# Optimization experiments

Hardware: AMD Instinct MI355X
Metric: run time of the kernel (lower is better)

Reference implementation:

```python
import jax, jax.numpy as jnp
import numpy as np

C = 384; H = 32; W = 32; HEADS = 12; HD = C // HEADS; MLP = 1536
KOFF = 5; OFF_RANGE = 2.0


def layer_norm(x, g, b, eps=1e-5):
    mu = jnp.mean(x, axis=-1, keepdims=True)
    var = jnp.mean(jnp.square(x - mu), axis=-1, keepdims=True)
    return (x - mu) * jax.lax.rsqrt(var + eps) * g + b


def depthwise_conv(x, k):
    # x: (B,H,W,C), k: (kh,kw,1,C), SAME padding, groups=C
    return jax.lax.conv_general_dilated(
        x, k, window_strides=(1, 1), padding='SAME',
        dimension_numbers=('NHWC', 'HWIO', 'NHWC'), feature_group_count=C)


def grid_sample_bilinear(img, pos):
    # img: (B,H,W,C); pos: (B,H,W,2) normalized (y,x) in [-1,1], align_corners=True, border clamp
    B, Hh, Ww, Cc = img.shape
    py = (pos[..., 0] + 1.0) * 0.5 * (Hh - 1)
    px = (pos[..., 1] + 1.0) * 0.5 * (Ww - 1)
    y0 = jnp.floor(py); x0 = jnp.floor(px)
    wy = (py - y0)[..., None]; wx = (px - x0)[..., None]
    y0i = jnp.clip(y0.astype(jnp.int32), 0, Hh - 1)
    y1i = jnp.clip(y0i + 1, 0, Hh - 1)
    x0i = jnp.clip(x0.astype(jnp.int32), 0, Ww - 1)
    x1i = jnp.clip(x0i + 1, 0, Ww - 1)
    b = jnp.arange(B)[:, None, None]
    g = lambda yi, xi: img[b, yi, xi]
    return (g(y0i, x0i) * (1 - wy) * (1 - wx) + g(y0i, x1i) * (1 - wy) * wx
            + g(y1i, x0i) * wy * (1 - wx) + g(y1i, x1i) * wy * wx)


def setup_inputs() -> dict:
    key = jax.random.key(0)
    ks = jax.random.split(key, 16)
    n = jax.random.normal
    s = 0.02
    inp = {
        'x': n(ks[0], (16, H * W, C), jnp.float32),
        'ln1_g': jnp.ones((C,), jnp.float32), 'ln1_b': jnp.zeros((C,), jnp.float32),
        'Wq': n(ks[1], (C, C), jnp.float32) * s, 'bq': jnp.zeros((C,), jnp.float32),
        'off_k': n(ks[2], (KOFF, KOFF, 1, C), jnp.float32) * s,
        'off_kb': jnp.zeros((C,), jnp.float32),
        'offln_g': jnp.ones((C,), jnp.float32), 'offln_b': jnp.zeros((C,), jnp.float32),
        'Woff': n(ks[3], (2, C), jnp.float32) * s, 'boff': jnp.zeros((2,), jnp.float32),
        'Wk': n(ks[4], (C, C), jnp.float32) * s, 'bk': jnp.zeros((C,), jnp.float32),
        'Wv': n(ks[5], (C, C), jnp.float32) * s, 'bv': jnp.zeros((C,), jnp.float32),
        'Wo': n(ks[6], (C, C), jnp.float32) * s, 'bo': jnp.zeros((C,), jnp.float32),
        'ln2_g': jnp.ones((C,), jnp.float32), 'ln2_b': jnp.zeros((C,), jnp.float32),
        'W1': n(ks[7], (MLP, C), jnp.float32) * s, 'b1': jnp.zeros((MLP,), jnp.float32),
        'W2': n(ks[8], (C, MLP), jnp.float32) * s, 'b2': jnp.zeros((C,), jnp.float32),
    }
    return inp


def _block(x, ln1_g, ln1_b, Wq, bq, off_k, off_kb, offln_g, offln_b, Woff, boff,
           Wk, bk, Wv, bv, Wo, bo, ln2_g, ln2_b, W1, b1, W2, b2):
    B, N, _ = x.shape
    # --- deformable attention branch ---
    xn = layer_norm(x, ln1_g, ln1_b)
    xi = xn.reshape(B, H, W, C)
    q = xi @ Wq.T + bq                                  # (B,H,W,C)
    # offset network: depthwise conv -> LN -> GELU -> 1x1 conv to 2
    off = depthwise_conv(q, off_k) + off_kb
    off = jax.nn.gelu(layer_norm(off, offln_g, offln_b))
    off = off @ Woff.T + boff                           # (B,H,W,2)
    off_range = jnp.array([OFF_RANGE * 2.0 / H, OFF_RANGE * 2.0 / W], jnp.float32)
    off = jnp.tanh(off) * off_range                     # normalized coord units
    ry = (jnp.arange(H, dtype=jnp.float32) + 0.5) / H * 2.0 - 1.0
    rx = (jnp.arange(W, dtype=jnp.float32) + 0.5) / W * 2.0 - 1.0
    ref = jnp.stack(jnp.meshgrid(ry, rx, indexing='ij'), axis=-1)  # (H,W,2)
    pos = ref[None] + off                               # (B,H,W,2)
    xs = grid_sample_bilinear(xi, pos).reshape(B, N, C)  # sampled keys/values source
    k = xs @ Wk.T + bk
    v = xs @ Wv.T + bv
    qh = q.reshape(B, N, HEADS, HD).transpose(0, 2, 1, 3)
    kh = k.reshape(B, N, HEADS, HD).transpose(0, 2, 1, 3)
    vh = v.reshape(B, N, HEADS, HD).transpose(0, 2, 1, 3)
    attn = jax.nn.softmax(jnp.einsum('bhqd,bhkd->bhqk', qh, kh) * (HD ** -0.5), axis=-1)
    o = jnp.einsum('bhqk,bhkd->bhqd', attn, vh).transpose(0, 2, 1, 3).reshape(B, N, C)
    x = x + (o @ Wo.T + bo)
    # --- MLP branch ---
    y = layer_norm(x, ln2_g, ln2_b)
    y = jax.nn.gelu(y @ W1.T + b1) @ W2.T + b2
    return x + y


def reference(x, ln1_g, ln1_b, Wq, bq, off_k, off_kb, offln_g, offln_b, Woff, boff,
              Wk, bk, Wv, bv, Wo, bo, ln2_g, ln2_b, W1, b1, W2, b2):
    return _block(x, ln1_g, ln1_b, Wq, bq, off_k, off_kb, offln_g, offln_b, Woff, boff,
                  Wk, bk, Wv, bv, Wo, bo, ln2_g, ln2_b, W1, b1, W2, b2)
```

## Files before the change

### kernel.cpp

```cpp
#include <hip/hip_runtime.h>
#include <math.h>

#define DI __device__ __forceinline__

typedef __attribute__((ext_vector_type(8))) short bf16x8;
typedef __attribute__((ext_vector_type(4))) float f32x4;

static constexpr int CC = 384;
static constexpr float QSCALE = 0.17677669529663687f * 1.4426950408889634f;
static constexpr float INVQS  = 1.0f / QSCALE;

DI unsigned short f2bf(float f){
  unsigned u = __float_as_uint(f);
  u += 0x7FFFu + ((u >> 16) & 1u);
  return (unsigned short)(u >> 16);
}
DI float bf2f(unsigned short u){ return __uint_as_float((unsigned)u << 16); }
DI float lo16(unsigned u){ return __uint_as_float(u << 16); }
DI float hi16(unsigned u){ return __uint_as_float(u & 0xFFFF0000u); }
DI float fexp2(float x){ return __builtin_amdgcn_exp2f(x); }
DI float frcp(float x){ return __builtin_amdgcn_rcpf(x); }
DI float tanh_fast(float z){ return 1.f - 2.f*frcp(fexp2(2.8853900817779268f*z) + 1.f); }
DI float gelu_fast(float v){
  float u = v*v;
  float z = 0.7978845608028654f * fmaf(0.044715f*u, v, v);
  return v - v*frcp(fexp2(2.8853900817779268f*z) + 1.f);
}
DI f32x4 mfma16(bf16x8 a, bf16x8 b, f32x4 c){
  return __builtin_amdgcn_mfma_f32_16x16x32_bf16(a, b, c, 0, 0, 0);
}
DI void gload16(const unsigned short* g, unsigned short* l){
  __builtin_amdgcn_global_load_lds(
      (const __attribute__((address_space(1))) unsigned int*)(const void*)g,
      (__attribute__((address_space(3))) unsigned int*)(void*)l, 16, 0, 0);
}

__global__ __launch_bounds__(256) void k_cvt_all(
    const float* __restrict__ wq, const float* __restrict__ wk,
    const float* __restrict__ wv, const float* __restrict__ wo,
    const float* __restrict__ w1, const float* __restrict__ w2,
    const float* __restrict__ ofk,
    unsigned short* __restrict__ dst)
{
  int i4 = (blockIdx.x*256 + threadIdx.x)*4;
  if (i4 >= 1779072) return;
  const float* src; int off;
  if (i4 < 147456){ src = wq; off = i4; }
  else if (i4 < 294912){ src = wk; off = i4 - 147456; }
  else if (i4 < 442368){ src = wv; off = i4 - 294912; }
  else if (i4 < 589824){ src = wo; off = i4 - 442368; }
  else if (i4 < 1179648){ src = w1; off = i4 - 589824; }
  else if (i4 < 1769472){ src = w2; off = i4 - 1179648; }
  else { src = ofk; off = i4 - 1769472; }
  float4 v = *(const float4*)(src + off);
  uint2 o;
  o.x = ((unsigned)f2bf(v.y) << 16) | f2bf(v.x);
  o.y = ((unsigned)f2bf(v.w) << 16) | f2bf(v.z);
  *(uint2*)(dst + i4) = o;
}

template<int BIN>
__global__ __launch_bounds__(256) void k_ln(const float* __restrict__ xf,
    const unsigned short* __restrict__ xb,
    const float* __restrict__ g, const float* __restrict__ b,
    unsigned short* __restrict__ outb)
{
  int row = blockIdx.x*4 + (threadIdx.x >> 6);
  int l = threadIdx.x & 63;
  float v[6]; int ch[6];
  if constexpr (BIN){
    int cA = 4*l, cB = 256 + 2*l;
    ch[0]=cA; ch[1]=cA+1; ch[2]=cA+2; ch[3]=cA+3; ch[4]=cB; ch[5]=cB+1;
    const unsigned short* xp = xb + (size_t)row * CC;
    uint2 u2 = *(const uint2*)(xp + cA);
    unsigned u1 = *(const unsigned*)(xp + cB);
    v[0]=lo16(u2.x); v[1]=hi16(u2.x); v[2]=lo16(u2.y); v[3]=hi16(u2.y);
    v[4]=lo16(u1);   v[5]=hi16(u1);
  } else {
    const float* xp = xf + (size_t)row * CC;
#pragma unroll
    for (int p = 0; p < 6; p++){ ch[p] = l + 64*p; v[p] = xp[ch[p]]; }
  }
  float s = 0.f, s2 = 0.f;
#pragma unroll
  for (int p = 0; p < 6; p++){ s += v[p]; s2 += v[p]*v[p]; }
#pragma unroll
  for (int m = 32; m; m >>= 1){ s += __shfl_xor(s, m); s2 += __shfl_xor(s2, m); }
  float mu = s * (1.f/CC);
  float var = s2 * (1.f/CC) - mu*mu;
  float rs = rsqrtf(var + 1e-5f);
  float o[6];
#pragma unroll
  for (int p = 0; p < 6; p++) o[p] = (v[p] - mu) * rs * g[ch[p]] + b[ch[p]];
  unsigned short* op = outb + (size_t)row*CC;
  if constexpr (BIN){
    uint2 st;
    st.x = ((unsigned)f2bf(o[1]) << 16) | f2bf(o[0]);
    st.y = ((unsigned)f2bf(o[3]) << 16) | f2bf(o[2]);
    *(uint2*)(op + ch[0]) = st;
    *(unsigned*)(op + ch[4]) = ((unsigned)f2bf(o[5]) << 16) | f2bf(o[4]);
  } else {
#pragma unroll
    for (int p = 0; p < 6; p++) op[ch[p]] = f2bf(o[p]);
  }
}

template<int EPI>
__global__ __launch_bounds__(256) void k_gemm64(
    const unsigned short* __restrict__ A, const unsigned short* __restrict__ W,
    const float* __restrict__ bias, const float* __restrict__ bias2,
    const float* __restrict__ res, const unsigned short* __restrict__ resb,
    float* __restrict__ outf, unsigned short* __restrict__ outb,
    unsigned short* __restrict__ outb2, int ntn, int N, int K)
{
  __shared__ unsigned short As[2][2048];
  __shared__ unsigned short Bs[2][4096];
  int bid = blockIdx.x;
  int cpx = gridDim.x >> 3;
  int id = (bid & 7)*cpx + (bid >> 3);
  int bn = (id % ntn) * 128;
  int bm = (id / ntn) * 64;
  int t = threadIdx.x;
  int w = t >> 6, l = t & 63;
  int g = l >> 4, ln = l & 15;
  int wm = w >> 1, wn = w & 1;
  f32x4 acc[2][4];
#pragma unroll
  for (int i = 0; i < 2; i++)
#pragma unroll
    for (int j = 0; j < 4; j++) acc[i][j] = (f32x4){0.f,0.f,0.f,0.f};
  int srow = t >> 2, slot = t & 3;
  int srowB = srow + 64;
  int cb0 = (slot ^ (srow  & 3) ^ ((srow  >> 2) & 3)) * 8;
  int cb1 = (slot ^ (srowB & 3) ^ ((srowB >> 2) & 3)) * 8;
  const unsigned short* Ap  = A + (size_t)(bm + srow)*K + cb0;
  const unsigned short* Wp0 = W + (size_t)(bn + srow)*K + cb0;
  const unsigned short* Wp1 = W + (size_t)(bn + srowB)*K + cb1;
  int NT = K >> 5;
  int wl = w*512;
  gload16(Ap,  &As[0][wl]);
  gload16(Wp0, &Bs[0][wl]);
  gload16(Wp1, &Bs[0][wl + 2048]);
  __syncthreads();
  for (int kt = 0; kt < NT; kt++){
    int cur = kt & 1;
    if (kt + 1 < NT){
      int k0 = (kt + 1) << 5;
      gload16(Ap  + k0, &As[cur ^ 1][wl]);
      gload16(Wp0 + k0, &Bs[cur ^ 1][wl]);
      gload16(Wp1 + k0, &Bs[cur ^ 1][wl + 2048]);
    }
    bf16x8 af[2], bf[4];
#pragma unroll
    for (int mi = 0; mi < 2; mi++){
      int row = wm*32 + mi*16 + ln;
      int sl = g ^ (row & 3) ^ ((row >> 2) & 3);
      af[mi] = *(const bf16x8*)((const char*)As[cur] + row*64 + sl*16);
    }
#pragma unroll
    for (int ni = 0; ni < 4; ni++){
      int row = wn*64 + ni*16 + ln;
      int sl = g ^ (row & 3) ^ ((row >> 2) & 3);
      bf[ni] = *(const bf16x8*)((const char*)Bs[cur] + row*64 + sl*16);
    }
#pragma unroll
    for (int mi = 0; mi < 2; mi++)
#pragma unroll
      for (int ni = 0; ni < 4; ni++)
        acc[mi][ni] = mfma16(af[mi], bf[ni], acc[mi][ni]);
    if (kt + 1 < NT) __syncthreads();
  }
#pragma unroll
  for (int mi = 0; mi < 2; mi++)
#pragma unroll
  for (int ni = 0; ni < 4; ni++){
    int col = bn + wn*64 + ni*16 + ln;
    float bv;
    if constexpr (EPI == 6) bv = col < 384 ? bias[col] : bias2[col - 384];
    else bv = bias[col];
#pragma unroll
    for (int i = 0; i < 4; i++){
      int row = bm + wm*32 + mi*16 + g*4 + i;
      float v = acc[mi][ni][i] + bv;
      if constexpr (EPI == 2){ v += res[(size_t)row*N + col]; outb[(size_t)row*N + col] = f2bf(v); }
      if constexpr (EPI == 7){ v += bf2f(resb[(size_t)row*N + col]); outf[(size_t)row*N + col] = v; }
      if constexpr (EPI == 3) v = gelu_fast(v);
      if constexpr (EPI == 0) outf[(size_t)row*N + col] = v;
      if constexpr (EPI == 1 || EPI == 3) outb[(size_t)row*N + col] = f2bf(v);
      if constexpr (EPI == 5) outb[(size_t)row*N + col] = f2bf(v * QSCALE);
      if constexpr (EPI == 6){
        if (col < 384){
          outb[(size_t)row*384 + col] = f2bf(v);
        } else {
          int c = col - 384;
          int bb = row >> 10, key = row & 1023, h = c >> 5, d = c & 31;
          int k6 = key & 63;
          int phys = (key & ~63) | ((k6 & 15) << 2) | (k6 >> 4);
          outb2[(size_t)(((bb*12 + h) << 5) + d)*1024 + phys] = f2bf(v);
        }
      }
    }
  }
}

__global__ __launch_bounds__(64) void k_offset_sample(
    const unsigned short* __restrict__ qs, const unsigned short* __restrict__ xnb,
    const unsigned short* __restrict__ okb,
    const float* __restrict__ offkb,
    const float* __restrict__ offg, const float* __restrict__ offb,
    const float* __restrict__ Woff, const float* __restrict__ boff,
    unsigned short* __restrict__ xsb)
{
  int blk = blockIdx.x;
  int pix = (blk & 7)*2048 + (blk >> 3);
  int b = pix >> 10, n = pix & 1023;
  int y = n >> 5, x = n & 31;
  int t = threadIdx.x;
  int c8 = (t < 48 ? t : 47) * 8;
  float act = t < 48 ? 1.f : 0.f;
  const unsigned short* qb = qs + (size_t)b*1024*CC;
  int ry[5], rx[5]; unsigned my[5], mx[5];
#pragma unroll
  for (int k = 0; k < 5; k++){
    int yy = y + k - 2, xx = x + k - 2;
    my[k] = (yy >= 0 && yy < 32) ? 0xFFFFFFFFu : 0u;
    mx[k] = (xx >= 0 && xx < 32) ? 0xFFFFFFFFu : 0u;
    int yc = yy < 0 ? 0 : (yy > 31 ? 31 : yy);
    int xc = xx < 0 ? 0 : (xx > 31 ? 31 : xx);
    ry[k] = yc*32*CC; rx[k] = xc*CC;
  }
  float a[8];
#pragma unroll
  for (int j = 0; j < 8; j++) a[j] = 0.f;
#pragma unroll
  for (int ky = 0; ky < 5; ky++)
#pragma unroll
  for (int kx = 0; kx < 5; kx++){
    int tap = ky*5 + kx;
    unsigned m = my[ky] & mx[kx];
    uint4 q4 = *(const uint4*)(qb + ry[ky] + rx[kx] + c8);
    uint4 w4 = *(const uint4*)(okb + tap*CC + c8);
    q4.x &= m; q4.y &= m; q4.z &= m; q4.w &= m;
    a[0] = fmaf(lo16(q4.x), lo16(w4.x), a[0]);
    a[1] = fmaf(hi16(q4.x), hi16(w4.x), a[1]);
    a[2] = fmaf(lo16(q4.y), lo16(w4.y), a[2]);
    a[3] = fmaf(hi16(q4.y), hi16(w4.y), a[3]);
    a[4] = fmaf(lo16(q4.z), lo16(w4.z), a[4]);
    a[5] = fmaf(hi16(q4.z), hi16(w4.z), a[5]);
    a[6] = fmaf(lo16(q4.w), lo16(w4.w), a[6]);
    a[7] = fmaf(hi16(q4.w), hi16(w4.w), a[7]);
  }
  float4 kbA = *(const float4*)(offkb + c8);
  float4 kbB = *(const float4*)(offkb + c8 + 4);
  float c[8];
  c[0] = act * fmaf(a[0], INVQS, kbA.x);
  c[1] = act * fmaf(a[1], INVQS, kbA.y);
  c[2] = act * fmaf(a[2], INVQS, kbA.z);
  c[3] = act * fmaf(a[3], INVQS, kbA.w);
  c[4] = act * fmaf(a[4], INVQS, kbB.x);
  c[5] = act * fmaf(a[5], INVQS, kbB.y);
  c[6] = act * fmaf(a[6], INVQS, kbB.z);
  c[7] = act * fmaf(a[7], INVQS, kbB.w);
  float s = 0.f, s2 = 0.f;
#pragma unroll
  for (int j = 0; j < 8; j++){ s += c[j]; s2 += c[j]*c[j]; }
#pragma unroll
  for (int m2 = 32; m2; m2 >>= 1){ s += __shfl_xor(s, m2); s2 += __shfl_xor(s2, m2); }
  float mu = s * (1.f/CC);
  float var = s2 * (1.f/CC) - mu*mu;
  float rs = rsqrtf(var + 1e-5f);
  float4 gA = *(const float4*)(offg + c8); float4 gB = *(const float4*)(offg + c8 + 4);
  float4 oA = *(const float4*)(offb + c8); float4 oB = *(const float4*)(offb + c8 + 4);
  float4 wA = *(const float4*)(Woff + c8); float4 wB = *(const float4*)(Woff + c8 + 4);
  float4 wC = *(const float4*)(Woff + CC + c8); float4 wD = *(const float4*)(Woff + CC + c8 + 4);
  float gg[8] = {gA.x,gA.y,gA.z,gA.w,gB.x,gB.y,gB.z,gB.w};
  float bb[8] = {oA.x,oA.y,oA.z,oA.w,oB.x,oB.y,oB.z,oB.w};
  float w0[8] = {wA.x,wA.y,wA.z,wA.w,wB.x,wB.y,wB.z,wB.w};
  float w1[8] = {wC.x,wC.y,wC.z,wC.w,wD.x,wD.y,wD.z,wD.w};
  float p0 = 0.f, p1 = 0.f;
#pragma unroll
  for (int j = 0; j < 8; j++){
    float v = gelu_fast((c[j] - mu)*rs*gg[j] + bb[j]) * act;
    p0 = fmaf(v, w0[j], p0);
    p1 = fmaf(v, w1[j], p1);
  }
#pragma unroll
  for (int m2 = 32; m2; m2 >>= 1){ p0 += __shfl_xor(p0, m2); p1 += __shfl_xor(p1, m2); }
  float offy = tanh_fast(p0 + boff[0]) * 0.125f;
  float offx = tanh_fast(p1 + boff[1]) * 0.125f;
  float py = ((y + 0.5f)/16.f - 1.f + offy + 1.f) * 0.5f * 31.f;
  float px = ((x + 0.5f)/16.f - 1.f + offx + 1.f) * 0.5f * 31.f;
  float y0f = floorf(py), x0f = floorf(px);
  float wy = py - y0f, wx = px - x0f;
  int y0 = (int)y0f, x0 = (int)x0f;
  y0 = y0 < 0 ? 0 : (y0 > 31 ? 31 : y0);
  x0 = x0 < 0 ? 0 : (x0 > 31 ? 31 : x0);
  int y1 = y0 + 1 > 31 ? 31 : y0 + 1;
  int x1 = x0 + 1 > 31 ? 31 : x0 + 1;
  const unsigned short* s00 = xnb + (size_t)(b*1024 + y0*32 + x0)*CC + c8;
  const unsigned short* s01 = xnb + (size_t)(b*1024 + y0*32 + x1)*CC + c8;
  const unsigned short* s10 = xnb + (size_t)(b*1024 + y1*32 + x0)*CC + c8;
  const unsigned short* s11 = xnb + (size_t)(b*1024 + y1*32 + x1)*CC + c8;
  float w00 = (1.f-wy)*(1.f-wx), w01 = (1.f-wy)*wx, w10 = wy*(1.f-wx), w11 = wy*wx;
  uint4 A0 = *(const uint4*)s00;
  uint4 A1 = *(const uint4*)s01;
  uint4 A2 = *(const uint4*)s10;
  uint4 A3 = *(const uint4*)s11;
  if (t < 48){
    float r[8];
    r[0] = w00*lo16(A0.x) + w01*lo16(A1.x) + w10*lo16(A2.x) + w11*lo16(A3.x);
    r[1] = w00*hi16(A0.x) + w01*hi16(A1.x) + w10*hi16(A2.x) + w11*hi16(A3.x);
    r[2] = w00*lo16(A0.y) + w01*lo16(A1.y) + w10*lo16(A2.y) + w11*lo16(A3.y);
    r[3] = w00*hi16(A0.y) + w01*hi16(A1.y) + w10*hi16(A2.y) + w11*hi16(A3.y);
    r[4] = w00*lo16(A0.z) + w01*lo16(A1.z) + w10*lo16(A2.z) + w11*lo16(A3.z);
    r[5] = w00*hi16(A0.z) + w01*hi16(A1.z) + w10*hi16(A2.z) + w11*hi16(A3.z);
    r[6] = w00*lo16(A0.w) + w01*lo16(A1.w) + w10*lo16(A2.w) + w11*lo16(A3.w);
    r[7] = w00*hi16(A0.w) + w01*hi16(A1.w) + w10*hi16(A2.w) + w11*hi16(A3.w);
    uint4 st;
    st.x = ((unsigned)f2bf(r[1]) << 16) | f2bf(r[0]);
    st.y = ((unsigned)f2bf(r[3]) << 16) | f2bf(r[2]);
    st.z = ((unsigned)f2bf(r[5]) << 16) | f2bf(r[4]);
    st.w = ((unsigned)f2bf(r[7]) << 16) | f2bf(r[6]);
    *(uint4*)(xsb + (size_t)(b*1024 + n)*CC + c8) = st;
  }
}

__global__ __launch_bounds__(256) void k_attn(
    const unsigned short* __restrict__ qs, const unsigned short* __restrict__ kb,
    const unsigned short* __restrict__ vt, unsigned short* __restrict__ ob)
{
  __shared__ unsigned short Ks[2][64][40];
  __shared__ unsigned short Vs[2][32][72];
  __shared__ unsigned short Ps[4][32][72];
  int blk = blockIdx.x;
  int sw = (blk & 7)*192 + (blk >> 3);
  int qt = sw & 7, h = (sw >> 3) % 12, b = sw / 96;
  int t = threadIdx.x;
  int w = t >> 6, l = t & 63;
  int g = l >> 4, ln = l & 15;
  int q0 = qt*128 + w*32;
  bf16x8 qa[2];
#pragma unroll
  for (int mi = 0; mi < 2; mi++)
    qa[mi] = *(const bf16x8*)&qs[(size_t)(b*1024 + q0 + mi*16 + ln)*CC + h*32 + g*8];
  f32x4 z = {0.f,0.f,0.f,0.f};
  f32x4 oacc[2][2]; oacc[0][0]=z; oacc[0][1]=z; oacc[1][0]=z; oacc[1][1]=z;
  float lsum[2][4] = {{0.f,0.f,0.f,0.f},{0.f,0.f,0.f,0.f}};
  int krow = t >> 2, kc = (t & 3)*8;
  int vdim = t >> 3, vc = (t & 7)*8;
  const unsigned short* kptr = kb + (size_t)(b*1024 + krow)*CC + h*32 + kc;
  const unsigned short* vptr = vt + (size_t)((b*12 + h)*32 + vdim)*1024 + vc;
  {
    uint4 kr = *(const uint4*)kptr;
    uint4 vr = *(const uint4*)vptr;
    *(uint4*)&Ks[0][krow][kc] = kr;
    *(uint4*)&Vs[0][vdim][vc] = vr;
  }
  __syncthreads();
  for (int kt = 0; kt < 16; kt++){
    int cur = kt & 1;
    uint4 kr2, vr2;
    if (kt < 15){
      int k0 = (kt + 1)*64;
      kr2 = *(const uint4*)(kptr + (size_t)k0*CC);
      vr2 = *(const uint4*)(vptr + k0);
    }
    bf16x8 kf[4];
#pragma unroll
    for (int nt = 0; nt < 4; nt++) kf[nt] = *(const bf16x8*)&Ks[cur][nt*16 + ln][g*8];
    f32x4 s[2][4];
    __builtin_amdgcn_s_setprio(1);
#pragma unroll
    for (int mi = 0; mi < 2; mi++)
#pragma unroll
      for (int nt = 0; nt < 4; nt++) s[mi][nt] = mfma16(qa[mi], kf[nt], z);
    __builtin_amdgcn_s_setprio(0);
#pragma unroll
    for (int mi = 0; mi < 2; mi++)
#pragma unroll
      for (int i = 0; i < 4; i++){
        float p0 = fexp2(s[mi][0][i]);
        float p1 = fexp2(s[mi][1][i]);
        float p2 = fexp2(s[mi][2][i]);
        float p3 = fexp2(s[mi][3][i]);
        lsum[mi][i] += (p0 + p1) + (p2 + p3);
        int prow = mi*16 + g*4 + i;
        uint2 pk;
        pk.x = __builtin_amdgcn_perm(__float_as_uint(p1), __float_as_uint(p0), 0x07060302u);
        pk.y = __builtin_amdgcn_perm(__float_as_uint(p3), __float_as_uint(p2), 0x07060302u);
        *(uint2*)&Ps[w][prow][ln*4] = pk;
      }
    __builtin_amdgcn_s_setprio(1);
#pragma unroll
    for (int k2 = 0; k2 < 2; k2++){
      bf16x8 va[2];
#pragma unroll
      for (int d2 = 0; d2 < 2; d2++) va[d2] = *(const bf16x8*)&Vs[cur][d2*16 + ln][k2*32 + g*8];
#pragma unroll
      for (int mi = 0; mi < 2; mi++){
        bf16x8 pf = *(const bf16x8*)&Ps[w][mi*16 + ln][k2*32 + g*8];
#pragma unroll
        for (int d2 = 0; d2 < 2; d2++) oacc[mi][d2] = mfma16(pf, va[d2], oacc[mi][d2]);
      }
    }
    __builtin_amdgcn_s_setprio(0);
    if (kt < 15){
      *(uint4*)&Ks[cur ^ 1][krow][kc] = kr2;
      *(uint4*)&Vs[cur ^ 1][vdim][vc] = vr2;
      __syncthreads();
    }
  }
#pragma unroll
  for (int mi = 0; mi < 2; mi++)
#pragma unroll
    for (int i = 0; i < 4; i++){
#pragma unroll
      for (int mk = 8; mk; mk >>= 1) lsum[mi][i] += __shfl_xor(lsum[mi][i], mk);
      lsum[mi][i] = 1.f / lsum[mi][i];
    }
#pragma unroll
  for (int mi = 0; mi < 2; mi++)
#pragma unroll
  for (int d2 = 0; d2 < 2; d2++)
#pragma unroll
  for (int i = 0; i < 4; i++){
    float v = oacc[mi][d2][i] * lsum[mi][i];
    int row = q0 + mi*16 + g*4 + i;
    ob[(size_t)(b*1024 + row)*CC + h*32 + d2*16 + ln] = f2bf(v);
  }
}

extern "C" void kernel_launch(void* const* d_in, const int* in_sizes, int n_in,
                              void* d_out, int out_size, void* d_ws, size_t ws_size,
                              hipStream_t stream)
{
  (void)in_sizes; (void)n_in; (void)out_size; (void)ws_size;
  const float* x     = (const float*)d_in[0];
  const float* ln1g  = (const float*)d_in[1];
  const float* ln1b  = (const float*)d_in[2];
  const float* Wq    = (const float*)d_in[3];
  const float* bq    = (const float*)d_in[4];
  const float* offk  = (const float*)d_in[5];
  const float* offkb = (const float*)d_in[6];
  const float* offg  = (const float*)d_in[7];
  const float* offb  = (const float*)d_in[8];
  const float* Woff  = (const float*)d_in[9];
  const float* boff  = (const float*)d_in[10];
  const float* Wk    = (const float*)d_in[11];
  const float* bk    = (const float*)d_in[12];
  const float* Wv    = (const float*)d_in[13];
  const float* bv    = (const float*)d_in[14];
  const float* Wo    = (const float*)d_in[15];
  const float* bo    = (const float*)d_in[16];
  const float* ln2g  = (const float*)d_in[17];
  const float* ln2b  = (const float*)d_in[18];
  const float* W1    = (const float*)d_in[19];
  const float* b1    = (const float*)d_in[20];
  const float* W2    = (const float*)d_in[21];
  const float* b2    = (const float*)d_in[22];

  char* ws = (char*)d_ws;
  unsigned short* X2B = (unsigned short*)ws;
  unsigned short* XSB = (unsigned short*)(ws + 25165824);
  unsigned short* KB  = (unsigned short*)(ws + 37748736);
  unsigned short* VT  = (unsigned short*)(ws + 50331648);
  unsigned short* OB  = (unsigned short*)(ws + 62914560);
  unsigned short* XNB = (unsigned short*)(ws + 75497472);
  unsigned short* QSB = (unsigned short*)(ws + 88080384);
  unsigned short* YB  = QSB;
  unsigned short* HB  = (unsigned short*)(ws + 25165824);
  unsigned short* WQB = (unsigned short*)(ws + 100663296);
  unsigned short* WKB = WQB + 147456;
  unsigned short* WOB = WKB + 294912;
  unsigned short* W1B = WOB + 147456;
  unsigned short* W2B = W1B + 589824;
  unsigned short* OKB = W2B + 589824;

  k_cvt_all<<<1738, 256, 0, stream>>>(Wq, Wk, Wv, Wo, W1, W2, offk, WQB);
  k_ln<0><<<4096, 256, 0, stream>>>(x, nullptr, ln1g, ln1b, XNB);
  k_gemm64<5><<<768, 256, 0, stream>>>(XNB, WQB, bq, nullptr, nullptr, nullptr, nullptr, QSB, nullptr, 3, 384, 384);
  k_offset_sample<<<16384, 64, 0, stream>>>(QSB, XNB, OKB, offkb, offg, offb, Woff, boff, XSB);
  k_gemm64<6><<<1536, 256, 0, stream>>>(XSB, WKB, bk, bv, nullptr, nullptr, nullptr, KB, VT, 6, 768, 384);
  k_attn<<<1536, 256, 0, stream>>>(QSB, KB, VT, OB);
  k_gemm64<2><<<768, 256, 0, stream>>>(OB, WOB, bo, nullptr, x, nullptr, nullptr, X2B, nullptr, 3, 384, 384);
  k_ln<1><<<4096, 256, 0, stream>>>(nullptr, X2B, ln2g, ln2b, YB);
  k_gemm64<3><<<3072, 256, 0, stream>>>(YB, W1B, b1, nullptr, nullptr, nullptr, nullptr, HB, nullptr, 12, 1536, 384);
  k_gemm64<7><<<768, 256, 0, stream>>>(HB, W2B, b2, nullptr, nullptr, X2B, (float*)d_out, nullptr, nullptr, 3, 384, 1536);
}
```

Before: 245.1 us.

## Add 128x128 tiled MLP1 GEMM kernel and compute softmax row sums via MFMA

Replaces the generic 64-tile GEMM for the first MLP projection with a dedicated 128x128-tile kernel. It uses swizzled LDS double buffering via gload16 and a fused bias+GELU epilogue, aiming for more data reuse per tile and fewer blocks. In attention, the per-lane exp sums plus shuffle reduction are replaced by an extra MFMA against a ones vector, so row sums come from the bf16-rounded P values. This adds MFMA work but removes VALU adds and cross-lane shuffles, and uses an approximate reciprocal.

```diff
diff --git a/kernel.cpp b/kernel.cpp
--- a/kernel.cpp
+++ b/kernel.cpp
@@ -199,6 +199,84 @@
           outb2[(size_t)(((bb*12 + h) << 5) + d)*1024 + phys] = f2bf(v);
         }
       }
+    }
+  }
+}
+
+__global__ __launch_bounds__(256) void k_mlp1(
+    const unsigned short* __restrict__ A, const unsigned short* __restrict__ W,
+    const float* __restrict__ bias, unsigned short* __restrict__ outb)
+{
+  __shared__ unsigned short As[2][4096];
+  __shared__ unsigned short Bs[2][4096];
+  int bid = blockIdx.x;
+  int cpx = gridDim.x >> 3;
+  int id = (bid & 7)*cpx + (bid >> 3);
+  int bn = (id % 12) * 128;
+  int bm = (id / 12) * 128;
+  int t = threadIdx.x;
+  int w = t >> 6, l = t & 63;
+  int g = l >> 4, ln = l & 15;
+  int wm = w >> 1, wn = w & 1;
+  f32x4 acc[4][4];
+#pragma unroll
+  for (int i = 0; i < 4; i++)
+#pragma unroll
+    for (int j = 0; j < 4; j++) acc[i][j] = (f32x4){0.f,0.f,0.f,0.f};
+  int srow0 = t >> 2, slot = t & 3;
+  int srow1 = srow0 + 64;
+  int cb0 = (slot ^ (srow0 & 3) ^ ((srow0 >> 2) & 3)) * 8;
+  int cb1 = (slot ^ (srow1 & 3) ^ ((srow1 >> 2) & 3)) * 8;
+  const unsigned short* Ap0 = A + (size_t)(bm + srow0)*384 + cb0;
+  const unsigned short* Ap1 = A + (size_t)(bm + srow1)*384 + cb1;
+  const unsigned short* Wp0 = W + (size_t)(bn + srow0)*384 + cb0;
+  const unsigned short* Wp1 = W + (size_t)(bn + srow1)*384 + cb1;
+  int wl = w*512;
+  gload16(Ap0, &As[0][wl]);
+  gload16(Ap1, &As[0][wl + 2048]);
+  gload16(Wp0, &Bs[0][wl]);
+  gload16(Wp1, &Bs[0][wl + 2048]);
+  __syncthreads();
+  for (int kt = 0; kt < 12; kt++){
+    int cur = kt & 1;
+    if (kt < 11){
+      int k0 = (kt + 1) << 5;
+      gload16(Ap0 + k0, &As[cur ^ 1][wl]);
+      gload16(Ap1 + k0, &As[cur ^ 1][wl + 2048]);
+      gload16(Wp0 + k0, &Bs[cur ^ 1][wl]);
+      gload16(Wp1 + k0, &Bs[cur ^ 1][wl + 2048]);
+    }
+    bf16x8 af[4], bf[4];
+#pragma unroll
+    for (int mi = 0; mi < 4; mi++){
+      int row = wm*64 + mi*16 + ln;
+      int sl = g ^ (row & 3) ^ ((row >> 2) & 3);
+      af[mi] = *(const bf16x8*)((const char*)As[cur] + row*64 + sl*16);
+    }
+#pragma unroll
+    for (int ni = 0; ni < 4; ni++){
+      int row = wn*64 + ni*16 + ln;
+      int sl = g ^ (row & 3) ^ ((row >> 2) & 3);
+      bf[ni] = *(const bf16x8*)((const char*)Bs[cur] + row*64 + sl*16);
+    }
+#pragma unroll
+    for (int mi = 0; mi < 4; mi++)
+#pragma unroll
+      for (int ni = 0; ni < 4; ni++)
+        acc[mi][ni] = mfma16(af[mi], bf[ni], acc[mi][ni]);
+    if (kt < 11) __syncthreads();
+  }
+#pragma unroll
+  for (int mi = 0; mi < 4; mi++)
+#pragma unroll
+  for (int ni = 0; ni < 4; ni++){
+    int col = bn + wn*64 + ni*16 + ln;
+    float bv = bias[col];
+#pragma unroll
+    for (int i = 0; i < 4; i++){
+      int row = bm + wm*64 + mi*16 + g*4 + i;
+      float v = gelu_fast(acc[mi][ni][i] + bv);
+      outb[(size_t)row*1536 + col] = f2bf(v);
     }
   }
 }
@@ -343,9 +421,12 @@
 #pragma unroll
   for (int mi = 0; mi < 2; mi++)
     qa[mi] = *(const bf16x8*)&qs[(size_t)(b*1024 + q0 + mi*16 + ln)*CC + h*32 + g*8];
+  bf16x8 vones;
+#pragma unroll
+  for (int j = 0; j < 8; j++) vones[j] = (short)0x3F80;
   f32x4 z = {0.f,0.f,0.f,0.f};
   f32x4 oacc[2][2]; oacc[0][0]=z; oacc[0][1]=z; oacc[1][0]=z; oacc[1][1]=z;
-  float lsum[2][4] = {{0.f,0.f,0.f,0.f},{0.f,0.f,0.f,0.f}};
+  f32x4 lacc[2]; lacc[0]=z; lacc[1]=z;
   int krow = t >> 2, kc = (t & 3)*8;
   int vdim = t >> 3, vc = (t & 7)*8;
   const unsigned short* kptr = kb + (size_t)(b*1024 + krow)*CC + h*32 + kc;
@@ -383,7 +464,6 @@
         float p1 = fexp2(s[mi][1][i]);
         float p2 = fexp2(s[mi][2][i]);
         float p3 = fexp2(s[mi][3][i]);
-        lsum[mi][i] += (p0 + p1) + (p2 + p3);
         int prow = mi*16 + g*4 + i;
         uint2 pk;
         pk.x = __builtin_amdgcn_perm(__float_as_uint(p1), __float_as_uint(p0), 0x07060302u);
@@ -401,6 +481,7 @@
         bf16x8 pf = *(const bf16x8*)&Ps[w][mi*16 + ln][k2*32 + g*8];
 #pragma unroll
         for (int d2 = 0; d2 < 2; d2++) oacc[mi][d2] = mfma16(pf, va[d2], oacc[mi][d2]);
+        lacc[mi] = mfma16(pf, vones, lacc[mi]);
       }
     }
     __builtin_amdgcn_s_setprio(0);
@@ -410,21 +491,18 @@
       __syncthreads();
     }
   }
+  float rinv[2][4];
 #pragma unroll
   for (int mi = 0; mi < 2; mi++)
 #pragma unroll
-    for (int i = 0; i < 4; i++){
-#pragma unroll
-      for (int mk = 8; mk; mk >>= 1) lsum[mi][i] += __shfl_xor(lsum[mi][i], mk);
-      lsum[mi][i] = 1.f / lsum[mi][i];
-    }
+    for (int i = 0; i < 4; i++) rinv[mi][i] = frcp(lacc[mi][i]);
 #pragma unroll
   for (int mi = 0; mi < 2; mi++)
 #pragma unroll
   for (int d2 = 0; d2 < 2; d2++)
 #pragma unroll
   for (int i = 0; i < 4; i++){
-    float v = oacc[mi][d2][i] * lsum[mi][i];
+    float v = oacc[mi][d2][i] * rinv[mi][i];
     int row = q0 + mi*16 + g*4 + i;
     ob[(size_t)(b*1024 + row)*CC + h*32 + d2*16 + ln] = f2bf(v);
   }
@@ -484,6 +562,6 @@
   k_attn<<<1536, 256, 0, stream>>>(QSB, KB, VT, OB);
   k_gemm64<2><<<768, 256, 0, stream>>>(OB, WOB, bo, nullptr, x, nullptr, nullptr, X2B, nullptr, 3, 384, 384);
   k_ln<1><<<4096, 256, 0, stream>>>(nullptr, X2B, ln2g, ln2b, YB);
-  k_gemm64<3><<<3072, 256, 0, stream>>>(YB, W1B, b1, nullptr, nullptr, nullptr, nullptr, HB, nullptr, 12, 1536, 384);
+  k_mlp1<<<1536, 256, 0, stream>>>(YB, W1B, b1, HB);
   k_gemm64<7><<<768, 256, 0, stream>>>(HB, W2B, b2, nullptr, nullptr, X2B, (float*)d_out, nullptr, nullptr, 3, 384, 1536);
 }
```

New measurement: 240.3 us. -2.0%, faster.
